# Optimization experiments

Hardware: AMD Instinct MI355X
Metric: run time of the kernel (lower is better)

Reference implementation:

```python
import jax, jax.numpy as jnp
import numpy as np

BATCH = 8192
GROUPS = 512
ARITY = 3
OUT_DIM = 16
N_VERTS = 3 ** ARITY  # 27


def setup_inputs() -> dict:
    key = jax.random.key(0)
    k1, k2 = jax.random.split(key)
    # inputs in [-1, 1], the natural domain of the {-1,0,1}^arity grid
    X = jax.random.uniform(k1, (BATCH, GROUPS * ARITY), dtype=jnp.float32) * 2.0 - 1.0
    params = jax.random.uniform(k2, (GROUPS, N_VERTS, OUT_DIM), dtype=jnp.float32) * 2.0 - 1.0
    # center vertex (all-zero coordinate) pinned to 0, as in __init__
    params = params.at[:, (N_VERTS - 1) // 2, :].set(0.0)
    return {"X": X, "params": params}


def _interp(X, params):
    # X: [B, G*arity], params: [G, 3^arity, O]
    B = X.shape[0]
    G, V, O = params.shape
    arity = X.shape[1] // G
    X1 = X.reshape(B, G, arity)
    # piecewise-linear hat basis over grid points {-1, 0, +1} per dimension;
    # index d in {0,1,2} corresponds to coord d-1, matching vertex id
    # sum_j (x_j + 1) * 3^j from _compute_vertex_id.
    W = jnp.stack(
        [jax.nn.relu(-X1), 1.0 - jnp.abs(X1), jax.nn.relu(X1)], axis=-1
    )  # [B, G, arity, 3]
    # tensor-product basis over all 3^arity vertices, flattened so that
    # dimension j contributes d_j * 3^j (dim 0 least significant)
    basis = jnp.ones((B, G, 1), dtype=X.dtype)
    for j in range(arity - 1, -1, -1):
        basis = (basis[:, :, :, None] * W[:, :, j, None, :]).reshape(B, G, -1)
    # basis: [B, G, 3^arity]; weighted sum over vertex params
    out = jnp.einsum("bgv,gvo->bgo", basis, params)  # [B, G, O]
    return out.reshape(B, G * O)


def reference(X, params):
    return _interp(X, params)
```

## Files before the change

### kernel.cpp

```cpp
#include <hip/hip_runtime.h>

#define BATCH   8192
#define GROUPS  512
#define ARITY   3
#define OUT_DIM 16
#define NV      27
#define XCOLS   (GROUPS*ARITY)
#define OCOLS   (GROUPS*OUT_DIM)

#define BTILE 32
#define GTILE 16
#define PSTRIDE 444

typedef float    f32x4 __attribute__((ext_vector_type(4)));
typedef unsigned u32x2 __attribute__((ext_vector_type(2)));

__device__ __forceinline__ unsigned cvt_pk_bf16(float lo, float hi) {
    unsigned r;
    asm("v_cvt_pk_bf16_f32 %0, %1, %2" : "=v"(r) : "v"(lo), "v"(hi));
    return r;
}
__device__ __forceinline__ float bflo(unsigned u) {
    union { unsigned u; float f; } c; c.u = u << 16; return c.f;
}
__device__ __forceinline__ float bfhi(unsigned u) {
    union { unsigned u; float f; } c; c.u = u & 0xffff0000u; return c.f;
}

__global__ __launch_bounds__(256, 8) void lattice_interp_kernel(
    const float* __restrict__ X,
    const float* __restrict__ P,
    float* __restrict__ out)
{
    __shared__ float xs[BTILE * GTILE * ARITY];
    __shared__ unsigned short ps[GTILE * PSTRIDE];

    const int t  = threadIdx.x;
    const int b0 = blockIdx.y * BTILE;
    const int g0 = blockIdx.x * GTILE;

    {
        const float* src_base = X + (size_t)b0 * XCOLS + g0 * ARITY;
        #pragma unroll
        for (int k = 0; k < 2; ++k) {
            const int f = t + k * 256;
            if (f < 384) {
                const int r = f / 12, c = f % 12;
                const float* src = src_base + (size_t)r * XCOLS + c * 4;
                __builtin_amdgcn_global_load_lds(
                    (const __attribute__((address_space(1))) void*)src,
                    (__attribute__((address_space(3))) void*)&xs[f * 4],
                    16, 0, 0);
            }
        }
    }

    {
        const float4* src = reinterpret_cast<const float4*>(P + (size_t)g0 * (NV * OUT_DIM));
        #pragma unroll
        for (int k = 0; k < 7; ++k) {
            const int f = t + k * 256;
            if (f < 1728) {
                const float4 v = src[f];
                const int pgl = f / 108;
                const int rem = f - pgl * 108;
                u32x2 w;
                w.x = cvt_pk_bf16(v.x, v.y);
                w.y = cvt_pk_bf16(v.z, v.w);
                *reinterpret_cast<u32x2*>(&ps[pgl * PSTRIDE + rem * 4]) = w;
            }
        }
    }

    __syncthreads();

    const int wv = t >> 6;
    const int l  = t & 63;
    const int gl = l >> 2;
    const int oq = l & 3;

    const unsigned short* pbase = ps + gl * PSTRIDE + oq * 4;
    const float* xb = xs + gl * ARITY;
    float* outp = out + (size_t)b0 * OCOLS + (size_t)g0 * OUT_DIM + l * 4;

    #pragma unroll 2
    for (int i = 0; i < 8; ++i) {
        const int b = wv * 8 + i;
        const float x0 = xb[b * (GTILE * ARITY) + 0];
        const float x1 = xb[b * (GTILE * ARITY) + 1];
        const float x2 = xb[b * (GTILE * ARITY) + 2];

        const bool n0 = x0 < 0.0f, n1 = x1 < 0.0f, n2 = x2 < 0.0f;
        const float wl0 = n0 ? -x0       : 1.0f - x0;
        const float wh0 = n0 ? 1.0f + x0 : x0;
        const float wl1 = n1 ? -x1       : 1.0f - x1;
        const float wh1 = n1 ? 1.0f + x1 : x1;
        const float wl2 = n2 ? -x2       : 1.0f - x2;
        const float wh2 = n2 ? 1.0f + x2 : x2;
        const int   vb  = (n0 ? 0 : 1) + 3 * (n1 ? 0 : 1) + 9 * (n2 ? 0 : 1);

        const float wA = wl0 * wl1, wB = wh0 * wl1, wC = wl0 * wh1, wD = wh0 * wh1;
        const float c000 = wA * wl2, c100 = wB * wl2, c010 = wC * wl2, c110 = wD * wl2;
        const float c001 = wA * wh2, c101 = wB * wh2, c011 = wC * wh2, c111 = wD * wh2;

        const u32x2* pp = reinterpret_cast<const u32x2*>(pbase + (size_t)vb * 16);
        const u32x2 r0 = pp[0];
        const u32x2 r1 = pp[4];
        const u32x2 r2 = pp[12];
        const u32x2 r3 = pp[16];
        const u32x2 r4 = pp[36];
        const u32x2 r5 = pp[40];
        const u32x2 r6 = pp[48];
        const u32x2 r7 = pp[52];

        f32x4 acc;
        {
            f32x4 pv = { bflo(r0.x), bfhi(r0.x), bflo(r0.y), bfhi(r0.y) };
            acc = c000 * pv;
        }
        { f32x4 pv = { bflo(r1.x), bfhi(r1.x), bflo(r1.y), bfhi(r1.y) }; acc += c100 * pv; }
        { f32x4 pv = { bflo(r2.x), bfhi(r2.x), bflo(r2.y), bfhi(r2.y) }; acc += c010 * pv; }
        { f32x4 pv = { bflo(r3.x), bfhi(r3.x), bflo(r3.y), bfhi(r3.y) }; acc += c110 * pv; }
        { f32x4 pv = { bflo(r4.x), bfhi(r4.x), bflo(r4.y), bfhi(r4.y) }; acc += c001 * pv; }
        { f32x4 pv = { bflo(r5.x), bfhi(r5.x), bflo(r5.y), bfhi(r5.y) }; acc += c101 * pv; }
        { f32x4 pv = { bflo(r6.x), bfhi(r6.x), bflo(r6.y), bfhi(r6.y) }; acc += c011 * pv; }
        { f32x4 pv = { bflo(r7.x), bfhi(r7.x), bflo(r7.y), bfhi(r7.y) }; acc += c111 * pv; }

        __builtin_nontemporal_store(acc,
            reinterpret_cast<f32x4*>(outp + (size_t)b * OCOLS));
    }
}

extern "C" void kernel_launch(void* const* d_in, const int* in_sizes, int n_in,
                              void* d_out, int out_size, void* d_ws, size_t ws_size,
                              hipStream_t stream) {
    const float* X = (const float*)d_in[0];
    const float* P = (const float*)d_in[1];
    float* out = (float*)d_out;

    dim3 grid(GROUPS / GTILE, BATCH / BTILE);
    dim3 block(256);
    lattice_interp_kernel<<<grid, block, 0, stream>>>(X, P, out);
}
```

Before: 62.49 us.

## Process several batch chunks per block to reuse staged params

Each block now handles four consecutive 32-row batch chunks. It loads and converts the group's params to bf16 in LDS once, then loops over the chunks, reloading X for each into a single LDS buffer with barriers in between. This amortizes the params load and conversion over more rows and cuts the grid size by four. In exchange it adds serialized X loads and extra barriers between chunks with no double buffering, and there are fewer blocks to hide latency.

```diff
diff --git a/kernel.cpp b/kernel.cpp
--- a/kernel.cpp
+++ b/kernel.cpp
@@ -9,6 +9,7 @@
 #define OCOLS   (GROUPS*OUT_DIM)
 
 #define BTILE 32
+#define NCHUNK 4
 #define GTILE 16
 #define PSTRIDE 444
 
@@ -36,24 +37,8 @@
     __shared__ unsigned short ps[GTILE * PSTRIDE];
 
     const int t  = threadIdx.x;
-    const int b0 = blockIdx.y * BTILE;
     const int g0 = blockIdx.x * GTILE;
-
-    {
-        const float* src_base = X + (size_t)b0 * XCOLS + g0 * ARITY;
-        #pragma unroll
-        for (int k = 0; k < 2; ++k) {
-            const int f = t + k * 256;
-            if (f < 384) {
-                const int r = f / 12, c = f % 12;
-                const float* src = src_base + (size_t)r * XCOLS + c * 4;
-                __builtin_amdgcn_global_load_lds(
-                    (const __attribute__((address_space(1))) void*)src,
-                    (__attribute__((address_space(3))) void*)&xs[f * 4],
-                    16, 0, 0);
-            }
-        }
-    }
+    const int bbase = blockIdx.y * (BTILE * NCHUNK);
 
     {
         const float4* src = reinterpret_cast<const float4*>(P + (size_t)g0 * (NV * OUT_DIM));
@@ -72,6 +57,21 @@
         }
     }
 
+    {
+        const float* src_base = X + (size_t)bbase * XCOLS + g0 * ARITY;
+        #pragma unroll
+        for (int k = 0; k < 2; ++k) {
+            const int f = t + k * 256;
+            if (f < 384) {
+                const int r = f / 12, c = f % 12;
+                __builtin_amdgcn_global_load_lds(
+                    (const __attribute__((address_space(1))) void*)(src_base + (size_t)r * XCOLS + c * 4),
+                    (__attribute__((address_space(3))) void*)&xs[f * 4],
+                    16, 0, 0);
+            }
+        }
+    }
+
     __syncthreads();
 
     const int wv = t >> 6;
@@ -81,53 +81,73 @@
 
     const unsigned short* pbase = ps + gl * PSTRIDE + oq * 4;
     const float* xb = xs + gl * ARITY;
-    float* outp = out + (size_t)b0 * OCOLS + (size_t)g0 * OUT_DIM + l * 4;
 
-    #pragma unroll 2
-    for (int i = 0; i < 8; ++i) {
-        const int b = wv * 8 + i;
-        const float x0 = xb[b * (GTILE * ARITY) + 0];
-        const float x1 = xb[b * (GTILE * ARITY) + 1];
-        const float x2 = xb[b * (GTILE * ARITY) + 2];
+    #pragma unroll 1
+    for (int j = 0; j < NCHUNK; ++j) {
+        const int b0 = bbase + j * BTILE;
+        float* outp = out + (size_t)b0 * OCOLS + (size_t)g0 * OUT_DIM + l * 4;
 
-        const bool n0 = x0 < 0.0f, n1 = x1 < 0.0f, n2 = x2 < 0.0f;
-        const float wl0 = n0 ? -x0       : 1.0f - x0;
-        const float wh0 = n0 ? 1.0f + x0 : x0;
-        const float wl1 = n1 ? -x1       : 1.0f - x1;
-        const float wh1 = n1 ? 1.0f + x1 : x1;
-        const float wl2 = n2 ? -x2       : 1.0f - x2;
-        const float wh2 = n2 ? 1.0f + x2 : x2;
-        const int   vb  = (n0 ? 0 : 1) + 3 * (n1 ? 0 : 1) + 9 * (n2 ? 0 : 1);
+        #pragma unroll 2
+        for (int i = 0; i < 8; ++i) {
+            const int b = wv * 8 + i;
+            const float x0 = xb[b * (GTILE * ARITY) + 0];
+            const float x1 = xb[b * (GTILE * ARITY) + 1];
+            const float x2 = xb[b * (GTILE * ARITY) + 2];
 
-        const float wA = wl0 * wl1, wB = wh0 * wl1, wC = wl0 * wh1, wD = wh0 * wh1;
-        const float c000 = wA * wl2, c100 = wB * wl2, c010 = wC * wl2, c110 = wD * wl2;
-        const float c001 = wA * wh2, c101 = wB * wh2, c011 = wC * wh2, c111 = wD * wh2;
+            const bool n0 = x0 < 0.0f, n1 = x1 < 0.0f, n2 = x2 < 0.0f;
+            const float wl0 = n0 ? -x0       : 1.0f - x0;
+            const float wh0 = n0 ? 1.0f + x0 : x0;
+            const float wl1 = n1 ? -x1       : 1.0f - x1;
+            const float wh1 = n1 ? 1.0f + x1 : x1;
+            const float wl2 = n2 ? -x2       : 1.0f - x2;
+            const float wh2 = n2 ? 1.0f + x2 : x2;
+            const int   vb  = (n0 ? 0 : 1) + 3 * (n1 ? 0 : 1) + 9 * (n2 ? 0 : 1);
 
-        const u32x2* pp = reinterpret_cast<const u32x2*>(pbase + (size_t)vb * 16);
-        const u32x2 r0 = pp[0];
-        const u32x2 r1 = pp[4];
-        const u32x2 r2 = pp[12];
-        const u32x2 r3 = pp[16];
-        const u32x2 r4 = pp[36];
-        const u32x2 r5 = pp[40];
-        const u32x2 r6 = pp[48];
-        const u32x2 r7 = pp[52];
+            const float wA = wl0 * wl1, wB = wh0 * wl1, wC = wl0 * wh1, wD = wh0 * wh1;
+            const float c000 = wA * wl2, c100 = wB * wl2, c010 = wC * wl2, c110 = wD * wl2;
+            const float c001 = wA * wh2, c101 = wB * wh2, c011 = wC * wh2, c111 = wD * wh2;
 
-        f32x4 acc;
-        {
-            f32x4 pv = { bflo(r0.x), bfhi(r0.x), bflo(r0.y), bfhi(r0.y) };
-            acc = c000 * pv;
+            const u32x2* pp = reinterpret_cast<const u32x2*>(pbase + (size_t)vb * 16);
+            const u32x2 r0 = pp[0];
+            const u32x2 r1 = pp[4];
+            const u32x2 r2 = pp[12];
+            const u32x2 r3 = pp[16];
+            const u32x2 r4 = pp[36];
+            const u32x2 r5 = pp[40];
+            const u32x2 r6 = pp[48];
+            const u32x2 r7 = pp[52];
+
+            f32x4 acc;
+            { f32x4 pv = { bflo(r0.x), bfhi(r0.x), bflo(r0.y), bfhi(r0.y) }; acc  = c000 * pv; }
+            { f32x4 pv = { bflo(r1.x), bfhi(r1.x), bflo(r1.y), bfhi(r1.y) }; acc += c100 * pv; }
+            { f32x4 pv = { bflo(r2.x), bfhi(r2.x), bflo(r2.y), bfhi(r2.y) }; acc += c010 * pv; }
+            { f32x4 pv = { bflo(r3.x), bfhi(r3.x), bflo(r3.y), bfhi(r3.y) }; acc += c110 * pv; }
+            { f32x4 pv = { bflo(r4.x), bfhi(r4.x), bflo(r4.y), bfhi(r4.y) }; acc += c001 * pv; }
+            { f32x4 pv = { bflo(r5.x), bfhi(r5.x), bflo(r5.y), bfhi(r5.y) }; acc += c101 * pv; }
+            { f32x4 pv = { bflo(r6.x), bfhi(r6.x), bflo(r6.y), bfhi(r6.y) }; acc += c011 * pv; }
+            { f32x4 pv = { bflo(r7.x), bfhi(r7.x), bflo(r7.y), bfhi(r7.y) }; acc += c111 * pv; }
+
+            __builtin_nontemporal_store(acc,
+                reinterpret_cast<f32x4*>(outp + (size_t)b * OCOLS));
         }
-        { f32x4 pv = { bflo(r1.x), bfhi(r1.x), bflo(r1.y), bfhi(r1.y) }; acc += c100 * pv; }
-        { f32x4 pv = { bflo(r2.x), bfhi(r2.x), bflo(r2.y), bfhi(r2.y) }; acc += c010 * pv; }
-        { f32x4 pv = { bflo(r3.x), bfhi(r3.x), bflo(r3.y), bfhi(r3.y) }; acc += c110 * pv; }
-        { f32x4 pv = { bflo(r4.x), bfhi(r4.x), bflo(r4.y), bfhi(r4.y) }; acc += c001 * pv; }
-        { f32x4 pv = { bflo(r5.x), bfhi(r5.x), bflo(r5.y), bfhi(r5.y) }; acc += c101 * pv; }
-        { f32x4 pv = { bflo(r6.x), bfhi(r6.x), bflo(r6.y), bfhi(r6.y) }; acc += c011 * pv; }
-        { f32x4 pv = { bflo(r7.x), bfhi(r7.x), bflo(r7.y), bfhi(r7.y) }; acc += c111 * pv; }
 
-        __builtin_nontemporal_store(acc,
-            reinterpret_cast<f32x4*>(outp + (size_t)b * OCOLS));
+        __syncthreads();
+
+        if (j + 1 < NCHUNK) {
+            const float* src_base = X + (size_t)(bbase + (j + 1) * BTILE) * XCOLS + g0 * ARITY;
+            #pragma unroll
+            for (int k = 0; k < 2; ++k) {
+                const int f = t + k * 256;
+                if (f < 384) {
+                    const int r = f / 12, c = f % 12;
+                    __builtin_amdgcn_global_load_lds(
+                        (const __attribute__((address_space(1))) void*)(src_base + (size_t)r * XCOLS + c * 4),
+                        (__attribute__((address_space(3))) void*)&xs[f * 4],
+                        16, 0, 0);
+                }
+            }
+            __syncthreads();
+        }
     }
 }
 
@@ -138,7 +158,7 @@
     const float* P = (const float*)d_in[1];
     float* out = (float*)d_out;
 
-    dim3 grid(GROUPS / GTILE, BATCH / BTILE);
+    dim3 grid(GROUPS / GTILE, BATCH / (BTILE * NCHUNK));
     dim3 block(256);
     lattice_interp_kernel<<<grid, block, 0, stream>>>(X, P, out);
 }
```

Result: faster. 60.33 us, median of 2 (-3.5%).

## Grow batch tile per block and load X directly with register prefetch

Applied to the files above, without the earlier changes.

Each block now covers 128 batch rows instead of 32, so the bf16 parameter tile staged in LDS is reused across four times as many rows and the grid shrinks. X is no longer staged through LDS. Each lane reads its three inputs straight from global memory and prefetches the next row's values one iteration ahead. The trade is fewer blocks (less parallelism and tail balance) and scattered 12-byte global reads of X in place of coalesced LDS staging.

```diff
diff --git a/kernel.cpp b/kernel.cpp
--- a/kernel.cpp
+++ b/kernel.cpp
@@ -8,8 +8,8 @@
 #define XCOLS   (GROUPS*ARITY)
 #define OCOLS   (GROUPS*OUT_DIM)
 
-#define BTILE 32
 #define GTILE 16
+#define BROWS 128
 #define PSTRIDE 444
 
 typedef float    f32x4 __attribute__((ext_vector_type(4)));
@@ -32,28 +32,11 @@
     const float* __restrict__ P,
     float* __restrict__ out)
 {
-    __shared__ float xs[BTILE * GTILE * ARITY];
     __shared__ unsigned short ps[GTILE * PSTRIDE];
 
     const int t  = threadIdx.x;
-    const int b0 = blockIdx.y * BTILE;
     const int g0 = blockIdx.x * GTILE;
-
-    {
-        const float* src_base = X + (size_t)b0 * XCOLS + g0 * ARITY;
-        #pragma unroll
-        for (int k = 0; k < 2; ++k) {
-            const int f = t + k * 256;
-            if (f < 384) {
-                const int r = f / 12, c = f % 12;
-                const float* src = src_base + (size_t)r * XCOLS + c * 4;
-                __builtin_amdgcn_global_load_lds(
-                    (const __attribute__((address_space(1))) void*)src,
-                    (__attribute__((address_space(3))) void*)&xs[f * 4],
-                    16, 0, 0);
-            }
-        }
-    }
+    const int bbase = blockIdx.y * BROWS;
 
     {
         const float4* src = reinterpret_cast<const float4*>(P + (size_t)g0 * (NV * OUT_DIM));
@@ -80,23 +63,27 @@
     const int oq = l & 3;
 
     const unsigned short* pbase = ps + gl * PSTRIDE + oq * 4;
-    const float* xb = xs + gl * ARITY;
-    float* outp = out + (size_t)b0 * OCOLS + (size_t)g0 * OUT_DIM + l * 4;
+
+    const float* xrow = X + (size_t)(bbase + wv) * XCOLS + (size_t)(g0 + gl) * ARITY;
+    float* outp = out + (size_t)(bbase + wv) * OCOLS + (size_t)g0 * OUT_DIM + l * 4;
+
+    float x0 = xrow[0], x1 = xrow[1], x2 = xrow[2];
 
     #pragma unroll 2
-    for (int i = 0; i < 8; ++i) {
-        const int b = wv * 8 + i;
-        const float x0 = xb[b * (GTILE * ARITY) + 0];
-        const float x1 = xb[b * (GTILE * ARITY) + 1];
-        const float x2 = xb[b * (GTILE * ARITY) + 2];
+    for (int i = 0; i < BROWS / 4; ++i) {
+        const float cx0 = x0, cx1 = x1, cx2 = x2;
+        if (i + 1 < BROWS / 4) {
+            const float* nx = xrow + (size_t)(i + 1) * 4 * XCOLS;
+            x0 = nx[0]; x1 = nx[1]; x2 = nx[2];
+        }
 
-        const bool n0 = x0 < 0.0f, n1 = x1 < 0.0f, n2 = x2 < 0.0f;
-        const float wl0 = n0 ? -x0       : 1.0f - x0;
-        const float wh0 = n0 ? 1.0f + x0 : x0;
-        const float wl1 = n1 ? -x1       : 1.0f - x1;
-        const float wh1 = n1 ? 1.0f + x1 : x1;
-        const float wl2 = n2 ? -x2       : 1.0f - x2;
-        const float wh2 = n2 ? 1.0f + x2 : x2;
+        const bool n0 = cx0 < 0.0f, n1 = cx1 < 0.0f, n2 = cx2 < 0.0f;
+        const float wl0 = n0 ? -cx0       : 1.0f - cx0;
+        const float wh0 = n0 ? 1.0f + cx0 : cx0;
+        const float wl1 = n1 ? -cx1       : 1.0f - cx1;
+        const float wh1 = n1 ? 1.0f + cx1 : cx1;
+        const float wl2 = n2 ? -cx2       : 1.0f - cx2;
+        const float wh2 = n2 ? 1.0f + cx2 : cx2;
         const int   vb  = (n0 ? 0 : 1) + 3 * (n1 ? 0 : 1) + 9 * (n2 ? 0 : 1);
 
         const float wA = wl0 * wl1, wB = wh0 * wl1, wC = wl0 * wh1, wD = wh0 * wh1;
@@ -114,10 +101,7 @@
         const u32x2 r7 = pp[52];
 
         f32x4 acc;
-        {
-            f32x4 pv = { bflo(r0.x), bfhi(r0.x), bflo(r0.y), bfhi(r0.y) };
-            acc = c000 * pv;
-        }
+        { f32x4 pv = { bflo(r0.x), bfhi(r0.x), bflo(r0.y), bfhi(r0.y) }; acc  = c000 * pv; }
         { f32x4 pv = { bflo(r1.x), bfhi(r1.x), bflo(r1.y), bfhi(r1.y) }; acc += c100 * pv; }
         { f32x4 pv = { bflo(r2.x), bfhi(r2.x), bflo(r2.y), bfhi(r2.y) }; acc += c010 * pv; }
         { f32x4 pv = { bflo(r3.x), bfhi(r3.x), bflo(r3.y), bfhi(r3.y) }; acc += c110 * pv; }
@@ -127,7 +111,7 @@
         { f32x4 pv = { bflo(r7.x), bfhi(r7.x), bflo(r7.y), bfhi(r7.y) }; acc += c111 * pv; }
 
         __builtin_nontemporal_store(acc,
-            reinterpret_cast<f32x4*>(outp + (size_t)b * OCOLS));
+            reinterpret_cast<f32x4*>(outp + (size_t)i * 4 * OCOLS));
     }
 }
 
@@ -138,7 +122,7 @@
     const float* P = (const float*)d_in[1];
     float* out = (float*)d_out;
 
-    dim3 grid(GROUPS / GTILE, BATCH / BTILE);
+    dim3 grid(GROUPS / GTILE, BATCH / BROWS);
     dim3 block(256);
     lattice_interp_kernel<<<grid, block, 0, stream>>>(X, P, out);
 }
```

Measured after the change: 61.76 us. No clear change (-1.2%).
